# Kernel optimization log

Hardware: AMD Instinct MI355X
Metric: run time of the kernel (lower is better)

Reference implementation:

```python
import jax, jax.numpy as jnp
import numpy as np

N = 50000
E = 1600000
IN = 128
HID = 128
OUT = 64
NL = 200000
NEG_SLOPE = 0.2


def _glorot(key, shape):
    fan_in, fan_out = shape[0], shape[-1]
    s = jnp.sqrt(6.0 / (fan_in + fan_out))
    return jax.random.uniform(key, shape, jnp.float32, -s, s)


def setup_inputs() -> dict:
    key = jax.random.key(0)
    ks = jax.random.split(key, 16)
    x = jax.random.normal(ks[0], (N, IN), jnp.float32)
    edge_index = jax.random.randint(ks[1], (2, E), 0, N, dtype=jnp.int32)
    edge_label_index = jax.random.randint(ks[2], (2, NL), 0, N, dtype=jnp.int32)
    return {
        "x": x,
        "edge_index": edge_index,
        "edge_label_index": edge_label_index,
        "W1": _glorot(ks[3], (IN, HID)),  "a1s": _glorot(ks[4], (HID,)),  "a1d": _glorot(ks[5], (HID,)),  "b1": jnp.zeros((HID,), jnp.float32),
        "W2": _glorot(ks[6], (HID, HID)), "a2s": _glorot(ks[7], (HID,)),  "a2d": _glorot(ks[8], (HID,)),  "b2": jnp.zeros((HID,), jnp.float32),
        "W3": _glorot(ks[9], (HID, HID)), "a3s": _glorot(ks[10], (HID,)), "a3d": _glorot(ks[11], (HID,)), "b3": jnp.zeros((HID,), jnp.float32),
        "W4": _glorot(ks[12], (HID, OUT)), "b4": jnp.zeros((OUT,), jnp.float32),
    }


def _add_self_loops(edge_index, n):
    loop = jnp.arange(n, dtype=edge_index.dtype)
    return jnp.concatenate([edge_index, jnp.stack([loop, loop])], axis=1)


def gat_conv(x, edge_index, W, a_s, a_d, b):
    """PyG GATConv, heads=1, add_self_loops=True: gather, LeakyReLU score,
    segment softmax over destination nodes, scatter-add aggregate."""
    n = x.shape[0]
    ei = _add_self_loops(edge_index, n)
    src, dst = ei[0], ei[1]
    h = x @ W                                    # [N, H]
    e = jax.nn.leaky_relu((h @ a_s)[src] + (h @ a_d)[dst], NEG_SLOPE)  # [E']
    m = jax.ops.segment_max(e, dst, num_segments=n)
    p = jnp.exp(e - m[dst])
    s = jax.ops.segment_sum(p, dst, num_segments=n)
    alpha = p / s[dst]                           # segment softmax
    out = jax.ops.segment_sum(h[src] * alpha[:, None], dst, num_segments=n)
    return out + b


def gcn_conv(x, edge_index, W, b):
    """PyG GCNConv: self-loops + symmetric degree normalization."""
    n = x.shape[0]
    ei = _add_self_loops(edge_index, n)
    src, dst = ei[0], ei[1]
    h = x @ W
    deg = jax.ops.segment_sum(jnp.ones(src.shape, h.dtype), dst, num_segments=n)
    dinv = jax.lax.rsqrt(deg)
    norm = dinv[src] * dinv[dst]                 # [E']
    out = jax.ops.segment_sum(h[src] * norm[:, None], dst, num_segments=n)
    return out + b


def reference(x, edge_index, edge_label_index,
              W1, a1s, a1d, b1, W2, a2s, a2d, b2,
              W3, a3s, a3d, b3, W4, b4):
    h = jax.nn.relu(gat_conv(x, edge_index, W1, a1s, a1d, b1))
    h = jax.nn.relu(gat_conv(h, edge_index, W2, a2s, a2d, b2))
    h = jax.nn.relu(gat_conv(h, edge_index, W3, a3s, a3d, b3))
    z = gcn_conv(h, edge_index, W4, b4)          # [N, OUT]
    # decode: dot product of endpoint embeddings -> link logits [NL]
    return (z[edge_label_index[0]] * z[edge_label_index[1]]).sum(axis=-1)
```

## Files before the change

### kernel.cpp

```cpp
#include <hip/hip_runtime.h>
#include <hip/hip_fp16.h>
#include <math.h>

#define NN   50000
#define NE   1600000
#define NLBL 200000
#define CAP  80
#define NEG  0.2f
#define NBK  196
#define CAPB 8800
#define CHK  4096
#define GBIN 391

typedef unsigned short u16;
typedef _Float16 half8 __attribute__((ext_vector_type(8)));
typedef float floatx4 __attribute__((ext_vector_type(4)));


__device__ void ph_bin(int blk, const int* __restrict__ ei,
                       int* __restrict__ gcnt, unsigned* __restrict__ bins) {
    __shared__ int cntL[NBK];
    __shared__ int offL[NBK];
    __shared__ int curL[NBK];
    __shared__ int curG[NBK];
    __shared__ unsigned stage[CHK];
    const int tid = threadIdx.x;
    const int e0 = blk * CHK + tid * 16;
    const bool act = (e0 + 15) < NE;

    unsigned pk[16];
    int bb[16];
    if (act) {
#pragma unroll
        for (int g = 0; g < 4; ++g) {
            int4 s4 = *(const int4*)&ei[e0 + g * 4];
            int4 d4 = *(const int4*)&ei[NE + e0 + g * 4];
            int sa[4] = {s4.x, s4.y, s4.z, s4.w};
            int da[4] = {d4.x, d4.y, d4.z, d4.w};
#pragma unroll
            for (int k = 0; k < 4; ++k) {
                int idx = g * 4 + k;
                bb[idx] = da[k] >> 8;
                pk[idx] = (unsigned)sa[k] | ((unsigned)(da[k] & 255) << 16)
                        | ((unsigned)bb[idx] << 24);
            }
        }
    }
    for (int i = tid; i < NBK; i += 256) cntL[i] = 0;
    __syncthreads();
    if (act) {
#pragma unroll
        for (int k = 0; k < 16; ++k) atomicAdd(&cntL[bb[k]], 1);
    }
    __syncthreads();
    if (tid < NBK) {
        int acc = 0;
        for (int i = 0; i < tid; ++i) acc += cntL[i];
        offL[tid] = acc;
        curL[tid] = acc;
    }
    __syncthreads();
    for (int i = tid; i < NBK; i += 256) curG[i] = atomicAdd(&gcnt[i], cntL[i]);
    __syncthreads();
    if (act) {
#pragma unroll
        for (int k = 0; k < 16; ++k) {
            int pos = atomicAdd(&curL[bb[k]], 1);
            stage[pos] = pk[k];
        }
    }
    __syncthreads();
    const int tot = offL[NBK - 1] + cntL[NBK - 1];
    for (int j = tid; j < tot; j += 256) {
        unsigned v = stage[j];
        int b = v >> 24;
        int lr = j - offL[b];
        bins[(size_t)b * CAPB + curG[b] + lr] = v & 0x00FFFFFFu;
    }
}

__global__ __launch_bounds__(256) void k_build(const unsigned* __restrict__ bins,
                                               const int* __restrict__ gcnt,
                                               int* __restrict__ cnt,
                                               u16* __restrict__ csr) {
    __shared__ u16 rows[256 * CAP];
    __shared__ int cur[256];
    const int b = blockIdx.x, tid = threadIdx.x;
    const int d0 = b << 8;
    const int nd = min(256, NN - d0);
    if (tid < nd) { cur[tid] = 1; rows[tid * CAP] = (u16)(d0 + tid); }
    __syncthreads();
    const int n = gcnt[b];
    for (int i = tid; i < n; i += 256) {
        unsigned v = bins[(size_t)b * CAPB + i];
        int s = v & 0xFFFF, dl = (v >> 16) & 0xFF;
        int pos = atomicAdd(&cur[dl], 1);
        if (pos < CAP) rows[dl * CAP + pos] = (u16)s;
    }
    __syncthreads();
    const unsigned* rw = (const unsigned*)rows;
    unsigned* cw = (unsigned*)(csr + (size_t)d0 * CAP);
    const int tot = nd * (CAP / 2);
    for (int i = tid; i < tot; i += 256) cw[i] = rw[i];
    if (tid < nd) cnt[d0 + tid] = cur[tid];
}


__global__ __launch_bounds__(256) void k_pre(const float* __restrict__ W1f,
                                             const float* __restrict__ W2f,
                                             const float* __restrict__ W3f,
                                             const float* __restrict__ W4f,
                                             half8* __restrict__ Wf1,
                                             half8* __restrict__ Wf2,
                                             half8* __restrict__ Wf3,
                                             half8* __restrict__ Wf4,
                                             int* __restrict__ gcnt) {
    if (blockIdx.x == 28) {
        int i = threadIdx.x;
        if (i < NBK) gcnt[i] = 0;
        return;
    }
    int e = blockIdx.x * 256 + threadIdx.x;
    const float* W;
    half8* Wf;
    int nout, le;
    if (e < 2048)      { W = W1f; Wf = Wf1; nout = 128; le = e; }
    else if (e < 4096) { W = W2f; Wf = Wf2; nout = 128; le = e - 2048; }
    else if (e < 6144) { W = W3f; Wf = Wf3; nout = 128; le = e - 4096; }
    else               { W = W4f; Wf = Wf4; nout = 64;  le = e - 6144; }
    int c = le >> 8, rem = le & 255, ks = rem >> 6, lane = rem & 63;
    int n = lane & 15, quad = lane >> 4;
    int col = c * 16 + n, k0 = ks * 32 + quad * 8;
    half8 v;
#pragma unroll
    for (int j = 0; j < 8; ++j) v[j] = (_Float16)W[(size_t)(k0 + j) * nout + col];
    Wf[le] = v;
}


template <int NOUT, bool ATTN, typename TA>
__device__ __forceinline__ void gemm_tile(int gt, int lane,
                                          const TA* __restrict__ A0,
                                          const TA* __restrict__ A1,
                                          const half8* __restrict__ Wf,
                                          __half* __restrict__ C0,
                                          __half* __restrict__ C1,
                                          const float* __restrict__ a_s,
                                          const float* __restrict__ a_d,
                                          float* __restrict__ asv,
                                          float* __restrict__ adv) {
    constexpr int CT = NOUT / 16;
    const int n = lane & 15, quad = lane >> 4;
    if (gt * 16 >= NN) return;
    const int row = gt * 16 + n;

    half8 a[4];
#pragma unroll
    for (int ks = 0; ks < 4; ++ks) {
        int c128 = ks * 32 + quad * 8;
        if constexpr (sizeof(TA) == 2) {
            const TA* Ah = (c128 < 64) ? A0 : A1;
            a[ks] = *(const half8*)((const _Float16*)Ah + (size_t)row * 64 + (c128 & 63));
        } else {
            const float* Ap = (const float*)A0 + (size_t)row * 128 + c128;
            float4 f0 = *(const float4*)Ap;
            float4 f1 = *(const float4*)(Ap + 4);
            half8 v;
            v[0] = (_Float16)f0.x; v[1] = (_Float16)f0.y; v[2] = (_Float16)f0.z; v[3] = (_Float16)f0.w;
            v[4] = (_Float16)f1.x; v[5] = (_Float16)f1.y; v[6] = (_Float16)f1.z; v[7] = (_Float16)f1.w;
            a[ks] = v;
        }
    }

    floatx4 acc[CT];
#pragma unroll
    for (int c = 0; c < CT; ++c) acc[c] = (floatx4){0.f, 0.f, 0.f, 0.f};
#pragma unroll
    for (int c = 0; c < CT; ++c) {
#pragma unroll
        for (int ks = 0; ks < 4; ++ks) {
            half8 b = Wf[(c * 4 + ks) * 64 + lane];
            acc[c] = __builtin_amdgcn_mfma_f32_16x16x32_f16(b, a[ks], acc[c], 0, 0, 0);
        }
    }

#pragma unroll
    for (int c = 0; c < CT; ++c) {
        __half* Ch = (NOUT == 64 || c < 4) ? C0 : C1;
        int coff = (NOUT == 64 || c < 4) ? c * 16 : (c - 4) * 16;
        __half2 h0 = __floats2half2_rn(acc[c][0], acc[c][1]);
        __half2 h1 = __floats2half2_rn(acc[c][2], acc[c][3]);
        uint2 u;
        __builtin_memcpy(&u.x, &h0, 4);
        __builtin_memcpy(&u.y, &h1, 4);
        *(uint2*)&Ch[(size_t)row * 64 + coff + quad * 4] = u;
    }

    if (ATTN) {
        float ps = 0.f, pd = 0.f;
#pragma unroll
        for (int c = 0; c < CT; ++c) {
#pragma unroll
            for (int reg = 0; reg < 4; ++reg) {
                float w = acc[c][reg];
                ps = fmaf(w, a_s[c * 16 + quad * 4 + reg], ps);
                pd = fmaf(w, a_d[c * 16 + quad * 4 + reg], pd);
            }
        }
        ps += __shfl_xor(ps, 16); ps += __shfl_xor(ps, 32);
        pd += __shfl_xor(pd, 16); pd += __shfl_xor(pd, 32);
        if (quad == 0) { asv[row] = ps; adv[row] = pd; }
    }
}

__global__ __launch_bounds__(256) void k_bin_gemm1(const int* __restrict__ ei,
                                                   int* __restrict__ gcnt,
                                                   unsigned* __restrict__ bins,
                                                   const float* __restrict__ x,
                                                   const half8* __restrict__ Wf1,
                                                   __half* __restrict__ G0,
                                                   __half* __restrict__ G1,
                                                   const float* __restrict__ a_s,
                                                   const float* __restrict__ a_d,
                                                   float* __restrict__ asv,
                                                   float* __restrict__ adv) {
    if (blockIdx.x < GBIN) { ph_bin(blockIdx.x, ei, gcnt, bins); return; }
    int gt = (blockIdx.x - GBIN) * 4 + (threadIdx.x >> 6);
    gemm_tile<128, true, float>(gt, threadIdx.x & 63, x, x, Wf1, G0, G1, a_s, a_d, asv, adv);
}

template <int NOUT, bool ATTN>
__global__ __launch_bounds__(64) void k_gemm64(const __half* __restrict__ A0,
                                               const __half* __restrict__ A1,
                                               const half8* __restrict__ Wf,
                                               __half* __restrict__ C0,
                                               __half* __restrict__ C1,
                                               const float* __restrict__ a_s,
                                               const float* __restrict__ a_d,
                                               float* __restrict__ asv,
                                               float* __restrict__ adv) {
    gemm_tile<NOUT, ATTN, __half>(blockIdx.x, threadIdx.x & 63, A0, A1, Wf, C0, C1,
                                  a_s, a_d, asv, adv);
}

__device__ __forceinline__ void fma_h8v(half8 h, float al, float* acc) {
#pragma unroll
    for (int k = 0; k < 8; ++k) acc[k] = fmaf(al, (float)h[k], acc[k]);
}


__global__ __launch_bounds__(256) void k_gat_agg(const __half* __restrict__ h0,
                                                 const __half* __restrict__ h1,
                                                 const int* __restrict__ cnt,
                                                 const u16* __restrict__ csr,
                                                 const float* __restrict__ asv,
                                                 const float* __restrict__ adv,
                                                 const float* __restrict__ bias,
                                                 __half* __restrict__ out0,
                                                 __half* __restrict__ out1) {
    __shared__ float alsL[4][88];
    __shared__ int   srcL[4][88];
    int lane = threadIdx.x & 63, wv = threadIdx.x >> 6;
    int d = blockIdx.x * 4 + wv;
    if (d >= NN) return;
    int deg = cnt[d]; if (deg > CAP) deg = CAP;
    const float advd = adv[d];
    const u16* rowp = csr + (size_t)d * CAP;

    int j0 = lane, j1 = lane + 64;
    int s0 = 0, s1 = 0;
    float e0 = -INFINITY, e1 = -INFINITY;
    if (j0 < deg) {
        s0 = rowp[j0];
        float t = asv[s0] + advd;
        e0 = (t >= 0.f) ? t : NEG * t;
    }
    if (j1 < deg) {
        s1 = rowp[j1];
        float t = asv[s1] + advd;
        e1 = (t >= 0.f) ? t : NEG * t;
    }
    float m = fmaxf(e0, e1);
#pragma unroll
    for (int off = 32; off; off >>= 1) m = fmaxf(m, __shfl_xor(m, off));
    float p0 = (j0 < deg) ? __expf(e0 - m) : 0.f;
    float p1 = (j1 < deg) ? __expf(e1 - m) : 0.f;
    float s = p0 + p1;
#pragma unroll
    for (int off = 32; off; off >>= 1) s += __shfl_xor(s, off);
    float inv = 1.f / s;
    alsL[wv][j0] = p0 * inv;
    srcL[wv][j0] = s0;
    if (j1 < 88) { alsL[wv][j1] = p1 * inv; srcL[wv][j1] = s1; }

    int slot = lane >> 3, r = lane & 7;
    int degp = (deg + 7) & ~7;
#pragma unroll
    for (int half = 0; half < 2; ++half) {
        const __half* ht = half ? h1 : h0;
        __half* ot = half ? out1 : out0;
        float acc[8];
#pragma unroll
        for (int k = 0; k < 8; ++k) acc[k] = 0.f;

        for (int base = 0; base < degp; base += 8) {
            int idx = base + slot;
            float al = alsL[wv][idx];
            int   sj = srcL[wv][idx];
            half8 hv = *(const half8*)&ht[(size_t)sj * 64 + r * 8];
            fma_h8v(hv, al, acc);
        }
#pragma unroll
        for (int k = 0; k < 8; ++k) {
            acc[k] += __shfl_xor(acc[k], 8);
            acc[k] += __shfl_xor(acc[k], 16);
            acc[k] += __shfl_xor(acc[k], 32);
        }
        if (slot == 0) {
            __half2 ho[4];
#pragma unroll
            for (int k = 0; k < 4; ++k) {
                float oa = fmaxf(acc[2 * k]     + bias[half * 64 + r * 8 + 2 * k],     0.f);
                float ob = fmaxf(acc[2 * k + 1] + bias[half * 64 + r * 8 + 2 * k + 1], 0.f);
                ho[k] = __floats2half2_rn(oa, ob);
            }
            uint4 u;
            __builtin_memcpy(&u, &ho[0], 16);
            *(uint4*)&ot[(size_t)d * 64 + r * 8] = u;
        }
    }
}


__global__ __launch_bounds__(256) void k_gcn_agg(const __half* __restrict__ h,
                                                 const int* __restrict__ cnt,
                                                 const u16* __restrict__ csr,
                                                 const float* __restrict__ bias,
                                                 __half* __restrict__ z) {
    __shared__ float nmL[4][88];
    __shared__ int   srcL[4][88];
    int lane = threadIdx.x & 63, wv = threadIdx.x >> 6;
    int d = blockIdx.x * 4 + wv;
    if (d >= NN) return;
    int degc = cnt[d];
    int deg = degc > CAP ? CAP : degc;
    float did = rsqrtf((float)degc);
    const u16* rowp = csr + (size_t)d * CAP;

    int j0 = lane, j1 = lane + 64;
    int s0 = 0, s1 = 0;
    float n0 = 0.f, n1 = 0.f;
    if (j0 < deg) { s0 = rowp[j0]; n0 = rsqrtf((float)cnt[s0]) * did; }
    if (j1 < deg) { s1 = rowp[j1]; n1 = rsqrtf((float)cnt[s1]) * did; }
    nmL[wv][j0] = n0;
    srcL[wv][j0] = s0;
    if (j1 < 88) { nmL[wv][j1] = n1; srcL[wv][j1] = s1; }

    int slot = lane >> 3, r = lane & 7;
    float acc[8];
#pragma unroll
    for (int k = 0; k < 8; ++k) acc[k] = 0.f;

    int degp = (deg + 7) & ~7;
    for (int base = 0; base < degp; base += 8) {
        int idx = base + slot;
        float nm = nmL[wv][idx];
        int   sj = srcL[wv][idx];
        half8 hv = *(const half8*)&h[(size_t)sj * 64 + r * 8];
        fma_h8v(hv, nm, acc);
    }
#pragma unroll
    for (int k = 0; k < 8; ++k) {
        acc[k] += __shfl_xor(acc[k], 8);
        acc[k] += __shfl_xor(acc[k], 16);
        acc[k] += __shfl_xor(acc[k], 32);
    }
    if (slot == 0) {
        __half2 ho[4];
#pragma unroll
        for (int k = 0; k < 4; ++k) {
            float oa = acc[2 * k]     + bias[r * 8 + 2 * k];
            float ob = acc[2 * k + 1] + bias[r * 8 + 2 * k + 1];
            ho[k] = __floats2half2_rn(oa, ob);
        }
        uint4 u;
        __builtin_memcpy(&u, &ho[0], 16);
        *(uint4*)&z[(size_t)d * 64 + r * 8] = u;
    }
}


__global__ __launch_bounds__(256) void k_decode(const __half* __restrict__ z,
                                                const int* __restrict__ eli,
                                                float* __restrict__ outp) {
    int lane = threadIdx.x & 63, wv = threadIdx.x >> 6;
    int g = lane >> 4, r = lane & 15;
    int idx = (blockIdx.x * 4 + wv) * 4 + g;
    if (idx >= NLBL) return;
    int a = eli[idx], b = eli[NLBL + idx];
    uint2 ua = *(const uint2*)&z[(size_t)a * 64 + r * 4];
    uint2 ub = *(const uint2*)&z[(size_t)b * 64 + r * 4];
    float2 a0 = __half22float2(*(__half2*)&ua.x);
    float2 a1 = __half22float2(*(__half2*)&ua.y);
    float2 b0 = __half22float2(*(__half2*)&ub.x);
    float2 b1 = __half22float2(*(__half2*)&ub.y);
    float v = a0.x * b0.x + a0.y * b0.y + a1.x * b1.x + a1.y * b1.y;
#pragma unroll
    for (int off = 8; off; off >>= 1) v += __shfl_xor(v, off);
    if (r == 0) outp[idx] = v;
}


extern "C" void kernel_launch(void* const* d_in, const int* in_sizes, int n_in,
                              void* d_out, int out_size, void* d_ws, size_t ws_size,
                              hipStream_t stream) {
    const float* x   = (const float*)d_in[0];
    const int*   ei  = (const int*)d_in[1];
    const int*   eli = (const int*)d_in[2];
    const float* W1 = (const float*)d_in[3];
    const float* a1s = (const float*)d_in[4];
    const float* a1d = (const float*)d_in[5];
    const float* b1 = (const float*)d_in[6];
    const float* W2 = (const float*)d_in[7];
    const float* a2s = (const float*)d_in[8];
    const float* a2d = (const float*)d_in[9];
    const float* b2 = (const float*)d_in[10];
    const float* W3 = (const float*)d_in[11];
    const float* a3s = (const float*)d_in[12];
    const float* a3d = (const float*)d_in[13];
    const float* b3 = (const float*)d_in[14];
    const float* W4 = (const float*)d_in[15];
    const float* b4 = (const float*)d_in[16];
    float* outp = (float*)d_out;

    char* p = (char*)d_ws;
    auto alloc = [&](size_t bytes) -> char* {
        char* r = p;
        p += (bytes + 255) & ~(size_t)255;
        return r;
    };
    int*    cnt  = (int*)alloc((size_t)NN * 4);
    u16*    csr  = (u16*)alloc((size_t)NN * CAP * 2);
    int*    gcnt = (int*)alloc((size_t)NBK * 4);
    float*  asv  = (float*)alloc((size_t)NN * 4);
    float*  advv = (float*)alloc((size_t)NN * 4);
    __half* G0   = (__half*)alloc((size_t)NN * 64 * 2);
    __half* G1   = (__half*)alloc((size_t)NN * 64 * 2);
    __half* B1a  = (__half*)alloc((size_t)NN * 64 * 2);
    __half* B1b  = (__half*)alloc((size_t)NN * 64 * 2);
    __half* B2a  = (__half*)alloc((size_t)NN * 64 * 2);
    __half* B2b  = (__half*)alloc((size_t)NN * 64 * 2);
    __half* zf   = (__half*)alloc((size_t)NN * 64 * 2);
    half8*  Wf1  = (half8*)alloc(2048 * 16);
    half8*  Wf2  = (half8*)alloc(2048 * 16);
    half8*  Wf3  = (half8*)alloc(2048 * 16);
    half8*  Wf4  = (half8*)alloc(1024 * 16);
    unsigned* bins = (unsigned*)alloc((size_t)NBK * CAPB * 4);

    const int gG1   = GBIN + 782;
    const int gGemm = (NN + 15) / 16;
    const int gNode = (NN + 3) / 4;
    const int gDec  = (NLBL + 15) / 16;

    k_pre<<<29, 256, 0, stream>>>(W1, W2, W3, W4, Wf1, Wf2, Wf3, Wf4, gcnt);
    k_bin_gemm1<<<gG1, 256, 0, stream>>>(ei, gcnt, bins, x, Wf1, G0, G1, a1s, a1d, asv, advv);
    k_build<<<NBK, 256, 0, stream>>>(bins, gcnt, cnt, csr);

    k_gat_agg<<<gNode, 256, 0, stream>>>(G0, G1, cnt, csr, asv, advv, b1, B1a, B1b);

    k_gemm64<128, true><<<gGemm, 64, 0, stream>>>(B1a, B1b, Wf2, G0, G1, a2s, a2d, asv, advv);
    k_gat_agg<<<gNode, 256, 0, stream>>>(G0, G1, cnt, csr, asv, advv, b2, B2a, B2b);

    k_gemm64<128, true><<<gGemm, 64, 0, stream>>>(B2a, B2b, Wf3, G0, G1, a3s, a3d, asv, advv);
    k_gat_agg<<<gNode, 256, 0, stream>>>(G0, G1, cnt, csr, asv, advv, b3, B1a, B1b);

    k_gemm64<64, false><<<gGemm, 64, 0, stream>>>(B1a, B1b, Wf4, G0, G0, nullptr, nullptr, nullptr, nullptr);
    k_gcn_agg<<<gNode, 256, 0, stream>>>(G0, cnt, csr, b4, zf);

    k_decode<<<gDec, 256, 0, stream>>>(zf, eli, outp);
}
```

Before: 369.9 us.

## Store hidden features as contiguous 128-wide rows and aggregate in one pass

Replaces the split pair of 64-column fp16 feature buffers with a single 128-column row-major buffer. The GAT aggregation can then gather a full 256-byte neighbor row in one pass, with 16 lanes per edge and 4 edges per step, instead of two half passes that each walk the neighbor list. Attention weight and source index are also packed into one float2 shared-memory entry, so each step needs one LDS read instead of two. Fewer edges run in parallel per step, so the loop has more iterations for the same degree.

```diff
diff --git a/kernel.cpp b/kernel.cpp
--- a/kernel.cpp
+++ b/kernel.cpp
@@ -140,16 +140,15 @@
 
 template <int NOUT, bool ATTN, typename TA>
 __device__ __forceinline__ void gemm_tile(int gt, int lane,
-                                          const TA* __restrict__ A0,
-                                          const TA* __restrict__ A1,
+                                          const TA* __restrict__ A,
                                           const half8* __restrict__ Wf,
-                                          __half* __restrict__ C0,
-                                          __half* __restrict__ C1,
+                                          __half* __restrict__ C,
                                           const float* __restrict__ a_s,
                                           const float* __restrict__ a_d,
                                           float* __restrict__ asv,
                                           float* __restrict__ adv) {
     constexpr int CT = NOUT / 16;
+    constexpr int OSTR = (NOUT == 64) ? 64 : 128;
     const int n = lane & 15, quad = lane >> 4;
     if (gt * 16 >= NN) return;
     const int row = gt * 16 + n;
@@ -159,10 +158,9 @@
     for (int ks = 0; ks < 4; ++ks) {
         int c128 = ks * 32 + quad * 8;
         if constexpr (sizeof(TA) == 2) {
-            const TA* Ah = (c128 < 64) ? A0 : A1;
-            a[ks] = *(const half8*)((const _Float16*)Ah + (size_t)row * 64 + (c128 & 63));
+            a[ks] = *(const half8*)((const _Float16*)A + (size_t)row * 128 + c128);
         } else {
-            const float* Ap = (const float*)A0 + (size_t)row * 128 + c128;
+            const float* Ap = (const float*)A + (size_t)row * 128 + c128;
             float4 f0 = *(const float4*)Ap;
             float4 f1 = *(const float4*)(Ap + 4);
             half8 v;
@@ -186,14 +184,12 @@
 
 #pragma unroll
     for (int c = 0; c < CT; ++c) {
-        __half* Ch = (NOUT == 64 || c < 4) ? C0 : C1;
-        int coff = (NOUT == 64 || c < 4) ? c * 16 : (c - 4) * 16;
         __half2 h0 = __floats2half2_rn(acc[c][0], acc[c][1]);
         __half2 h1 = __floats2half2_rn(acc[c][2], acc[c][3]);
         uint2 u;
         __builtin_memcpy(&u.x, &h0, 4);
         __builtin_memcpy(&u.y, &h1, 4);
-        *(uint2*)&Ch[(size_t)row * 64 + coff + quad * 4] = u;
+        *(uint2*)&C[(size_t)row * OSTR + c * 16 + quad * 4] = u;
     }
 
     if (ATTN) {
@@ -218,28 +214,25 @@
                                                    unsigned* __restrict__ bins,
                                                    const float* __restrict__ x,
                                                    const half8* __restrict__ Wf1,
-                                                   __half* __restrict__ G0,
-                                                   __half* __restrict__ G1,
+                                                   __half* __restrict__ G,
                                                    const float* __restrict__ a_s,
                                                    const float* __restrict__ a_d,
                                                    float* __restrict__ asv,
                                                    float* __restrict__ adv) {
     if (blockIdx.x < GBIN) { ph_bin(blockIdx.x, ei, gcnt, bins); return; }
     int gt = (blockIdx.x - GBIN) * 4 + (threadIdx.x >> 6);
-    gemm_tile<128, true, float>(gt, threadIdx.x & 63, x, x, Wf1, G0, G1, a_s, a_d, asv, adv);
+    gemm_tile<128, true, float>(gt, threadIdx.x & 63, x, Wf1, G, a_s, a_d, asv, adv);
 }
 
 template <int NOUT, bool ATTN>
-__global__ __launch_bounds__(64) void k_gemm64(const __half* __restrict__ A0,
-                                               const __half* __restrict__ A1,
+__global__ __launch_bounds__(64) void k_gemm64(const __half* __restrict__ A,
                                                const half8* __restrict__ Wf,
-                                               __half* __restrict__ C0,
-                                               __half* __restrict__ C1,
+                                               __half* __restrict__ C,
                                                const float* __restrict__ a_s,
                                                const float* __restrict__ a_d,
                                                float* __restrict__ asv,
                                                float* __restrict__ adv) {
-    gemm_tile<NOUT, ATTN, __half>(blockIdx.x, threadIdx.x & 63, A0, A1, Wf, C0, C1,
+    gemm_tile<NOUT, ATTN, __half>(blockIdx.x, threadIdx.x & 63, A, Wf, C,
                                   a_s, a_d, asv, adv);
 }
 
@@ -249,17 +242,14 @@
 }
 
 
-__global__ __launch_bounds__(256) void k_gat_agg(const __half* __restrict__ h0,
-                                                 const __half* __restrict__ h1,
+__global__ __launch_bounds__(256) void k_gat_agg(const __half* __restrict__ h,
                                                  const int* __restrict__ cnt,
                                                  const u16* __restrict__ csr,
                                                  const float* __restrict__ asv,
                                                  const float* __restrict__ adv,
                                                  const float* __restrict__ bias,
-                                                 __half* __restrict__ out0,
-                                                 __half* __restrict__ out1) {
-    __shared__ float alsL[4][88];
-    __shared__ int   srcL[4][88];
+                                                 __half* __restrict__ out) {
+    __shared__ float2 metaL[4][88];
     int lane = threadIdx.x & 63, wv = threadIdx.x >> 6;
     int d = blockIdx.x * 4 + wv;
     if (d >= NN) return;
@@ -289,45 +279,37 @@
 #pragma unroll
     for (int off = 32; off; off >>= 1) s += __shfl_xor(s, off);
     float inv = 1.f / s;
-    alsL[wv][j0] = p0 * inv;
-    srcL[wv][j0] = s0;
-    if (j1 < 88) { alsL[wv][j1] = p1 * inv; srcL[wv][j1] = s1; }
-
-    int slot = lane >> 3, r = lane & 7;
-    int degp = (deg + 7) & ~7;
-#pragma unroll
-    for (int half = 0; half < 2; ++half) {
-        const __half* ht = half ? h1 : h0;
-        __half* ot = half ? out1 : out0;
-        float acc[8];
-#pragma unroll
-        for (int k = 0; k < 8; ++k) acc[k] = 0.f;
-
-        for (int base = 0; base < degp; base += 8) {
-            int idx = base + slot;
-            float al = alsL[wv][idx];
-            int   sj = srcL[wv][idx];
-            half8 hv = *(const half8*)&ht[(size_t)sj * 64 + r * 8];
-            fma_h8v(hv, al, acc);
-        }
-#pragma unroll
-        for (int k = 0; k < 8; ++k) {
-            acc[k] += __shfl_xor(acc[k], 8);
-            acc[k] += __shfl_xor(acc[k], 16);
-            acc[k] += __shfl_xor(acc[k], 32);
-        }
-        if (slot == 0) {
-            __half2 ho[4];
-#pragma unroll
-            for (int k = 0; k < 4; ++k) {
-                float oa = fmaxf(acc[2 * k]     + bias[half * 64 + r * 8 + 2 * k],     0.f);
-                float ob = fmaxf(acc[2 * k + 1] + bias[half * 64 + r * 8 + 2 * k + 1], 0.f);
-                ho[k] = __floats2half2_rn(oa, ob);
-            }
-            uint4 u;
-            __builtin_memcpy(&u, &ho[0], 16);
-            *(uint4*)&ot[(size_t)d * 64 + r * 8] = u;
-        }
+    metaL[wv][j0] = make_float2(p0 * inv, __int_as_float(s0));
+    if (j1 < 88) metaL[wv][j1] = make_float2(p1 * inv, __int_as_float(s1));
+
+    int slot = lane >> 4, r = lane & 15;
+    float acc[8];
+#pragma unroll
+    for (int k = 0; k < 8; ++k) acc[k] = 0.f;
+    int degp = (deg + 3) & ~3;
+    for (int base = 0; base < degp; base += 4) {
+        float2 ms = metaL[wv][base + slot];
+        float al = ms.x;
+        int   sj = __float_as_int(ms.y);
+        half8 hv = *(const half8*)&h[(size_t)sj * 128 + r * 8];
+        fma_h8v(hv, al, acc);
+    }
+#pragma unroll
+    for (int k = 0; k < 8; ++k) {
+        acc[k] += __shfl_xor(acc[k], 16);
+        acc[k] += __shfl_xor(acc[k], 32);
+    }
+    if (slot == 0) {
+        __half2 ho[4];
+#pragma unroll
+        for (int k = 0; k < 4; ++k) {
+            float oa = fmaxf(acc[2 * k]     + bias[r * 8 + 2 * k],     0.f);
+            float ob = fmaxf(acc[2 * k + 1] + bias[r * 8 + 2 * k + 1], 0.f);
+            ho[k] = __floats2half2_rn(oa, ob);
+        }
+        uint4 u;
+        __builtin_memcpy(&u, &ho[0], 16);
+        *(uint4*)&out[(size_t)d * 128 + r * 8] = u;
     }
 }
 
@@ -337,8 +319,7 @@
                                                  const u16* __restrict__ csr,
                                                  const float* __restrict__ bias,
                                                  __half* __restrict__ z) {
-    __shared__ float nmL[4][88];
-    __shared__ int   srcL[4][88];
+    __shared__ float2 metaL[4][88];
     int lane = threadIdx.x & 63, wv = threadIdx.x >> 6;
     int d = blockIdx.x * 4 + wv;
     if (d >= NN) return;
@@ -352,9 +333,8 @@
     float n0 = 0.f, n1 = 0.f;
     if (j0 < deg) { s0 = rowp[j0]; n0 = rsqrtf((float)cnt[s0]) * did; }
     if (j1 < deg) { s1 = rowp[j1]; n1 = rsqrtf((float)cnt[s1]) * did; }
-    nmL[wv][j0] = n0;
-    srcL[wv][j0] = s0;
-    if (j1 < 88) { nmL[wv][j1] = n1; srcL[wv][j1] = s1; }
+    metaL[wv][j0] = make_float2(n0, __int_as_float(s0));
+    if (j1 < 88) metaL[wv][j1] = make_float2(n1, __int_as_float(s1));
 
     int slot = lane >> 3, r = lane & 7;
     float acc[8];
@@ -363,9 +343,9 @@
 
     int degp = (deg + 7) & ~7;
     for (int base = 0; base < degp; base += 8) {
-        int idx = base + slot;
-        float nm = nmL[wv][idx];
-        int   sj = srcL[wv][idx];
+        float2 ms = metaL[wv][base + slot];
+        float nm = ms.x;
+        int   sj = __float_as_int(ms.y);
         half8 hv = *(const half8*)&h[(size_t)sj * 64 + r * 8];
         fma_h8v(hv, nm, acc);
     }
@@ -444,18 +424,16 @@
     int*    gcnt = (int*)alloc((size_t)NBK * 4);
     float*  asv  = (float*)alloc((size_t)NN * 4);
     float*  advv = (float*)alloc((size_t)NN * 4);
-    __half* G0   = (__half*)alloc((size_t)NN * 64 * 2);
-    __half* G1   = (__half*)alloc((size_t)NN * 64 * 2);
-    __half* B1a  = (__half*)alloc((size_t)NN * 64 * 2);
-    __half* B1b  = (__half*)alloc((size_t)NN * 64 * 2);
-    __half* B2a  = (__half*)alloc((size_t)NN * 64 * 2);
-    __half* B2b  = (__half*)alloc((size_t)NN * 64 * 2);
+    __half* G    = (__half*)alloc((size_t)NN * 128 * 2);
+    __half* B1   = (__half*)alloc((size_t)NN * 128 * 2);
+    __half* B2   = (__half*)alloc((size_t)NN * 128 * 2);
     __half* zf   = (__half*)alloc((size_t)NN * 64 * 2);
     half8*  Wf1  = (half8*)alloc(2048 * 16);
     half8*  Wf2  = (half8*)alloc(2048 * 16);
     half8*  Wf3  = (half8*)alloc(2048 * 16);
     half8*  Wf4  = (half8*)alloc(1024 * 16);
     unsigned* bins = (unsigned*)alloc((size_t)NBK * CAPB * 4);
+    __half* H64  = B2;
 
     const int gG1   = GBIN + 782;
     const int gGemm = (NN + 15) / 16;
@@ -463,19 +441,19 @@
     const int gDec  = (NLBL + 15) / 16;
 
     k_pre<<<29, 256, 0, stream>>>(W1, W2, W3, W4, Wf1, Wf2, Wf3, Wf4, gcnt);
-    k_bin_gemm1<<<gG1, 256, 0, stream>>>(ei, gcnt, bins, x, Wf1, G0, G1, a1s, a1d, asv, advv);
+    k_bin_gemm1<<<gG1, 256, 0, stream>>>(ei, gcnt, bins, x, Wf1, G, a1s, a1d, asv, advv);
     k_build<<<NBK, 256, 0, stream>>>(bins, gcnt, cnt, csr);
 
-    k_gat_agg<<<gNode, 256, 0, stream>>>(G0, G1, cnt, csr, asv, advv, b1, B1a, B1b);
-
-    k_gemm64<128, true><<<gGemm, 64, 0, stream>>>(B1a, B1b, Wf2, G0, G1, a2s, a2d, asv, advv);
-    k_gat_agg<<<gNode, 256, 0, stream>>>(G0, G1, cnt, csr, asv, advv, b2, B2a, B2b);
-
-    k_gemm64<128, true><<<gGemm, 64, 0, stream>>>(B2a, B2b, Wf3, G0, G1, a3s, a3d, asv, advv);
-    k_gat_agg<<<gNode, 256, 0, stream>>>(G0, G1, cnt, csr, asv, advv, b3, B1a, B1b);
-
-    k_gemm64<64, false><<<gGemm, 64, 0, stream>>>(B1a, B1b, Wf4, G0, G0, nullptr, nullptr, nullptr, nullptr);
-    k_gcn_agg<<<gNode, 256, 0, stream>>>(G0, cnt, csr, b4, zf);
+    k_gat_agg<<<gNode, 256, 0, stream>>>(G, cnt, csr, asv, advv, b1, B1);
+
+    k_gemm64<128, true><<<gGemm, 64, 0, stream>>>(B1, Wf2, G, a2s, a2d, asv, advv);
+    k_gat_agg<<<gNode, 256, 0, stream>>>(G, cnt, csr, asv, advv, b2, B2);
+
+    k_gemm64<128, true><<<gGemm, 64, 0, stream>>>(B2, Wf3, G, a3s, a3d, asv, advv);
+    k_gat_agg<<<gNode, 256, 0, stream>>>(G, cnt, csr, asv, advv, b3, B1);
+
+    k_gemm64<64, false><<<gGemm, 64, 0, stream>>>(B1, Wf4, H64, nullptr, nullptr, nullptr, nullptr);
+    k_gcn_agg<<<gNode, 256, 0, stream>>>(H64, cnt, csr, b4, zf);
 
     k_decode<<<gDec, 256, 0, stream>>>(zf, eli, outp);
 }
```

Result: no change. 370.2 us (+0.1%).
